# Kernel tuning notes

Hardware: AMD Instinct MI355X
Metric: run time of the kernel (lower is better)

The kernel has to match this reference:

```python
import jax, jax.numpy as jnp
import numpy as np

CURV = 1.0          # Poincare ball curvature c
MIN_NORM = 1e-15    # clamp to avoid div-by-zero
TANH_CLIP = 1.0 - 1e-5  # keep artanh arg < 1


def _mobius_add(x, y, c):
    x2 = jnp.sum(x * x, axis=-1, keepdims=True)
    y2 = jnp.sum(y * y, axis=-1, keepdims=True)
    xy = jnp.sum(x * y, axis=-1, keepdims=True)
    num = (1.0 + 2.0 * c * xy + c * y2) * x + (1.0 - c * x2) * y
    den = 1.0 + 2.0 * c * xy + (c ** 2) * x2 * y2
    return num / jnp.maximum(den, MIN_NORM)


def _logmap(x, y, c):
    """Log map of y in the tangent space at x on the Poincare ball."""
    sub = _mobius_add(-x, y, c)
    sub_norm = jnp.maximum(jnp.linalg.norm(sub, axis=-1, keepdims=True), MIN_NORM)
    x2 = jnp.sum(x * x, axis=-1, keepdims=True)
    lam_x = 2.0 / jnp.maximum(1.0 - c * x2, MIN_NORM)
    sqrt_c = jnp.sqrt(c)
    arg = jnp.clip(sqrt_c * sub_norm, 0.0, TANH_CLIP)
    return (2.0 / (sqrt_c * lam_x)) * jnp.arctanh(arg) * sub / sub_norm


def _expmap(x, v, c):
    """Exp map of tangent vector v at point x on the Poincare ball."""
    v_norm = jnp.maximum(jnp.linalg.norm(v, axis=-1, keepdims=True), MIN_NORM)
    x2 = jnp.sum(x * x, axis=-1, keepdims=True)
    lam_x = 2.0 / jnp.maximum(1.0 - c * x2, MIN_NORM)
    sqrt_c = jnp.sqrt(c)
    second = jnp.tanh(sqrt_c * lam_x * v_norm / 2.0) * v / (sqrt_c * v_norm)
    return _mobius_add(x, second, c)


def setup_inputs() -> dict:
    key = jax.random.key(0)
    k1, k2, k3 = jax.random.split(key, 3)
    N, C_IN, C_OUT = 1536, 64, 64
    # points strictly inside the unit ball (norm ~0.25)
    x = jax.random.normal(k1, (N, C_IN), dtype=jnp.float32) * 0.03
    # Bernoulli(0.02) dense adjacency, float as in the torch module
    adj = (jax.random.uniform(k2, (N, N)) < 0.02).astype(jnp.float32)
    # kaiming-uniform-like init: U(-1/sqrt(fan_in), 1/sqrt(fan_in))
    bound = 1.0 / np.sqrt(C_IN)
    weight = jax.random.uniform(k3, (C_IN, C_OUT), dtype=jnp.float32,
                                minval=-bound, maxval=bound)
    bias = jnp.zeros((C_OUT,), dtype=jnp.float32)
    return {"x": x, "adj": adj, "weight": weight, "bias": bias}


def reference(x, adj, weight, bias):
    c = CURV
    # row-normalized aggregation weights
    deg = jnp.maximum(adj.sum(axis=1, keepdims=True), 1e-8)
    w = adj / deg                                   # (N, N)
    # pairwise logmap: tangent vector at node i pointing toward node j
    log_ij = _logmap(x[:, None, :], x[None, :, :], c)  # (N, N, C_in)
    agg = jnp.einsum('ij,ijc->ic', w, log_ij)          # (N, C_in)
    # (in_channels == out_channels here, so the torch pad/slice branch is a no-op)
    transformed = agg @ weight + bias                  # (N, C_out)
    origin = jnp.zeros_like(transformed)
    return _expmap(origin, transformed, c)
```

## Files before the change

kernel.cpp:

```cpp
#include <hip/hip_runtime.h>
#include <math.h>

#define NN 1536
#define CC 64
#define MAXP 160

__device__ __forceinline__ float wredsum64(float v) {
#pragma unroll
    for (int off = 32; off > 0; off >>= 1) v += __shfl_xor(v, off, 64);
    return v;
}

__launch_bounds__(256, 6)
__global__ void hmp_kernel(const float* __restrict__ x,
                           const float* __restrict__ adj,
                           const float* __restrict__ W,
                           const float* __restrict__ bias,
                           float* __restrict__ out) {
    const int i = blockIdx.x;
    const int tid = threadIdx.x;
    const int w = tid >> 6;
    const int lane = tid & 63;
    const int sub = tid & 15;
    const int g = tid >> 4;

    __shared__ int s_np;
    __shared__ int s_q[MAXP];
    __shared__ float s_qa[MAXP];
    __shared__ float s_part[16][CC];
    __shared__ float s_coefA[16];
    __shared__ float s_deg[4];
    __shared__ float s_agg[CC];
    __shared__ float s_t[4][CC];

    if (tid == 0) s_np = 0;

    const float4 xi4 = reinterpret_cast<const float4*>(x + (size_t)i * CC)[sub];
    const float4* arow4 = reinterpret_cast<const float4*>(adj + (size_t)i * NN);
    const float4 a0 = arow4[tid];
    float4 a1 = make_float4(0.f, 0.f, 0.f, 0.f);
    if (tid < 128) a1 = arow4[256 + tid];

    float a2 = xi4.x * xi4.x + xi4.y * xi4.y + xi4.z * xi4.z + xi4.w * xi4.w;
#pragma unroll
    for (int off = 1; off < 16; off <<= 1) a2 += __shfl_xor(a2, off, 64);
    const float B = 1.0f - a2;

    float degl = a0.x + a0.y + a0.z + a0.w + a1.x + a1.y + a1.z + a1.w;
    degl = wredsum64(degl);
    if (lane == 0) s_deg[w] = degl;

    __syncthreads();

    {
        const float va[8] = {a0.x, a0.y, a0.z, a0.w, a1.x, a1.y, a1.z, a1.w};
#pragma unroll
        for (int k = 0; k < 8; ++k) {
            const float v = va[k];
            if (v != 0.0f) {
                const int p = atomicAdd(&s_np, 1);
                if (p < MAXP) {
                    s_q[p] = (k < 4) ? (4 * tid + k) : (1024 + 4 * tid + (k - 4));
                    s_qa[p] = v;
                }
            }
        }
    }
    __syncthreads();
    const int np = min(s_np, MAXP);

    float accx = 0.f, accy = 0.f, accz = 0.f, accw = 0.f, coefA = 0.f;
    for (int p = g; p < np; p += 16) {
        const int j = s_q[p];
        const float aval = s_qa[p];
        const float4 xj4 = reinterpret_cast<const float4*>(x + (size_t)j * CC)[sub];
        float pd = xi4.x * xj4.x + xi4.y * xj4.y + xi4.z * xj4.z + xi4.w * xj4.w;
        float pb = xj4.x * xj4.x + xj4.y * xj4.y + xj4.z * xj4.z + xj4.w * xj4.w;
#pragma unroll
        for (int off = 1; off < 16; off <<= 1) {
            pd += __shfl_xor(pd, off, 64);
            pb += __shfl_xor(pb, off, 64);
        }
        const float dot = pd, b2 = pb;
        const float A = 1.0f - 2.0f * dot + b2;
        const float D = fmaxf(1.0f - 2.0f * dot + a2 * b2, 1e-15f);
        const float rD = 1.0f / D;
        const float num = fmaxf(A * A * a2 - 2.0f * A * B * dot + B * B * b2, 0.0f);
        const float sub2 = num * rD * rD;
        const float sn = fmaxf(sqrtf(sub2), 1e-15f);
        const float z = fminf(sn, 1.0f - 1e-5f);
        const float ath = 0.5f * logf((1.0f + z) / (1.0f - z));
        const float gg = aval * B * (ath / sn) * rD;
        coefA = fmaf(gg, A, coefA);
        const float gB = gg * B;
        accx = fmaf(gB, xj4.x, accx);
        accy = fmaf(gB, xj4.y, accy);
        accz = fmaf(gB, xj4.z, accz);
        accw = fmaf(gB, xj4.w, accw);
    }
    reinterpret_cast<float4*>(s_part[g])[sub] = make_float4(accx, accy, accz, accw);
    if (sub == 0) s_coefA[g] = coefA;
    __syncthreads();

    if (w == 0) {
        float acct = 0.f, coefAt = 0.f;
#pragma unroll
        for (int q = 0; q < 16; ++q) {
            acct += s_part[q][lane];
            coefAt += s_coefA[q];
        }
        const float deg = fmaxf(s_deg[0] + s_deg[1] + s_deg[2] + s_deg[3], 1e-8f);
        const float xl = x[(size_t)i * CC + lane];
        s_agg[lane] = (acct - xl * coefAt) / deg;
    }
    __syncthreads();

    {
        float t = 0.f;
        const int c0 = w * 16;
#pragma unroll
        for (int k = 0; k < 16; ++k) {
            t = fmaf(s_agg[c0 + k], W[(c0 + k) * CC + lane], t);
        }
        s_t[w][lane] = t;
    }
    __syncthreads();

    if (w == 0) {
        float t = bias[lane] + s_t[0][lane] + s_t[1][lane] + s_t[2][lane] + s_t[3][lane];
        const float vn2 = wredsum64(t * t);
        const float vn = fmaxf(sqrtf(vn2), 1e-15f);
        const float f = tanhf(vn) / vn;
        out[(size_t)i * CC + lane] = f * t;
    }
}

extern "C" void kernel_launch(void* const* d_in, const int* in_sizes, int n_in,
                              void* d_out, int out_size, void* d_ws, size_t ws_size,
                              hipStream_t stream) {
    const float* x    = (const float*)d_in[0];
    const float* adj  = (const float*)d_in[1];
    const float* W    = (const float*)d_in[2];
    const float* bias = (const float*)d_in[3];
    float* out = (float*)d_out;

    hmp_kernel<<<NN, 256, 0, stream>>>(x, adj, W, bias, out);
}
```

Before: 12.44 us.

## Unroll neighbor loop by two, prefetch weights, use fast intrinsics, drop a barrier

The neighbor loop now handles two neighbors per iteration so two gathers and their shuffle reductions can overlap. The weight matrix, bias and x row are loaded into registers at kernel start, before the adjacency scan. Every wave now computes the aggregated vector redundantly, and values are passed by lane shuffle instead of through shared memory, which removes one __syncthreads. Divisions, log and tanh are replaced with hardware reciprocal, __logf and an exp-based tanh, which trades some accuracy for fewer instructions.

```diff
diff --git a/kernel.cpp b/kernel.cpp
--- a/kernel.cpp
+++ b/kernel.cpp
@@ -4,6 +4,8 @@
 #define NN 1536
 #define CC 64
 #define MAXP 160
+
+#define RCP(x) __builtin_amdgcn_rcpf(x)
 
 __device__ __forceinline__ float wredsum64(float v) {
 #pragma unroll
@@ -30,16 +32,22 @@
     __shared__ float s_part[16][CC];
     __shared__ float s_coefA[16];
     __shared__ float s_deg[4];
-    __shared__ float s_agg[CC];
     __shared__ float s_t[4][CC];
 
     if (tid == 0) s_np = 0;
 
-    const float4 xi4 = reinterpret_cast<const float4*>(x + (size_t)i * CC)[sub];
     const float4* arow4 = reinterpret_cast<const float4*>(adj + (size_t)i * NN);
     const float4 a0 = arow4[tid];
     float4 a1 = make_float4(0.f, 0.f, 0.f, 0.f);
     if (tid < 128) a1 = arow4[256 + tid];
+
+    const float4 xi4 = reinterpret_cast<const float4*>(x + (size_t)i * CC)[sub];
+    const float xl = x[(size_t)i * CC + lane];
+    const float bi = bias[lane];
+
+    float wreg[16];
+#pragma unroll
+    for (int k = 0; k < 16; ++k) wreg[k] = W[(size_t)(w * 16 + k) * CC + lane];
 
     float a2 = xi4.x * xi4.x + xi4.y * xi4.y + xi4.z * xi4.z + xi4.w * xi4.w;
 #pragma unroll
@@ -70,68 +78,87 @@
     const int np = min(s_np, MAXP);
 
     float accx = 0.f, accy = 0.f, accz = 0.f, accw = 0.f, coefA = 0.f;
-    for (int p = g; p < np; p += 16) {
-        const int j = s_q[p];
-        const float aval = s_qa[p];
-        const float4 xj4 = reinterpret_cast<const float4*>(x + (size_t)j * CC)[sub];
-        float pd = xi4.x * xj4.x + xi4.y * xj4.y + xi4.z * xj4.z + xi4.w * xj4.w;
-        float pb = xj4.x * xj4.x + xj4.y * xj4.y + xj4.z * xj4.z + xj4.w * xj4.w;
+    for (int p = g; p < np; p += 32) {
+        const int p1 = p + 16;
+        const bool h1 = p1 < np;
+        const int j0 = s_q[p];
+        const float av0 = s_qa[p];
+        const int j1 = h1 ? s_q[p1] : j0;
+        const float av1 = h1 ? s_qa[p1] : 0.0f;
+
+        const float4 xa = reinterpret_cast<const float4*>(x + (size_t)j0 * CC)[sub];
+        const float4 xb = reinterpret_cast<const float4*>(x + (size_t)j1 * CC)[sub];
+
+        float pd0 = xi4.x * xa.x + xi4.y * xa.y + xi4.z * xa.z + xi4.w * xa.w;
+        float pb0 = xa.x * xa.x + xa.y * xa.y + xa.z * xa.z + xa.w * xa.w;
+        float pd1 = xi4.x * xb.x + xi4.y * xb.y + xi4.z * xb.z + xi4.w * xb.w;
+        float pb1 = xb.x * xb.x + xb.y * xb.y + xb.z * xb.z + xb.w * xb.w;
 #pragma unroll
         for (int off = 1; off < 16; off <<= 1) {
-            pd += __shfl_xor(pd, off, 64);
-            pb += __shfl_xor(pb, off, 64);
+            pd0 += __shfl_xor(pd0, off, 64);
+            pb0 += __shfl_xor(pb0, off, 64);
+            pd1 += __shfl_xor(pd1, off, 64);
+            pb1 += __shfl_xor(pb1, off, 64);
         }
-        const float dot = pd, b2 = pb;
-        const float A = 1.0f - 2.0f * dot + b2;
-        const float D = fmaxf(1.0f - 2.0f * dot + a2 * b2, 1e-15f);
-        const float rD = 1.0f / D;
-        const float num = fmaxf(A * A * a2 - 2.0f * A * B * dot + B * B * b2, 0.0f);
-        const float sub2 = num * rD * rD;
-        const float sn = fmaxf(sqrtf(sub2), 1e-15f);
-        const float z = fminf(sn, 1.0f - 1e-5f);
-        const float ath = 0.5f * logf((1.0f + z) / (1.0f - z));
-        const float gg = aval * B * (ath / sn) * rD;
-        coefA = fmaf(gg, A, coefA);
-        const float gB = gg * B;
-        accx = fmaf(gB, xj4.x, accx);
-        accy = fmaf(gB, xj4.y, accy);
-        accz = fmaf(gB, xj4.z, accz);
-        accw = fmaf(gB, xj4.w, accw);
+        {
+            const float A = 1.0f - 2.0f * pd0 + pb0;
+            const float D = fmaxf(1.0f - 2.0f * pd0 + a2 * pb0, 1e-15f);
+            const float rD = RCP(D);
+            const float num = fmaxf(A * A * a2 - 2.0f * A * B * pd0 + B * B * pb0, 0.0f);
+            const float sn = fmaxf(sqrtf(num) * rD, 1e-15f);
+            const float z = fminf(sn, 1.0f - 1e-5f);
+            const float ath = 0.5f * __logf((1.0f + z) * RCP(1.0f - z));
+            const float gg = av0 * B * ath * RCP(sn) * rD;
+            coefA = fmaf(gg, A, coefA);
+            const float gB = gg * B;
+            accx = fmaf(gB, xa.x, accx); accy = fmaf(gB, xa.y, accy);
+            accz = fmaf(gB, xa.z, accz); accw = fmaf(gB, xa.w, accw);
+        }
+        {
+            const float A = 1.0f - 2.0f * pd1 + pb1;
+            const float D = fmaxf(1.0f - 2.0f * pd1 + a2 * pb1, 1e-15f);
+            const float rD = RCP(D);
+            const float num = fmaxf(A * A * a2 - 2.0f * A * B * pd1 + B * B * pb1, 0.0f);
+            const float sn = fmaxf(sqrtf(num) * rD, 1e-15f);
+            const float z = fminf(sn, 1.0f - 1e-5f);
+            const float ath = 0.5f * __logf((1.0f + z) * RCP(1.0f - z));
+            const float gg = av1 * B * ath * RCP(sn) * rD;
+            coefA = fmaf(gg, A, coefA);
+            const float gB = gg * B;
+            accx = fmaf(gB, xb.x, accx); accy = fmaf(gB, xb.y, accy);
+            accz = fmaf(gB, xb.z, accz); accw = fmaf(gB, xb.w, accw);
+        }
     }
     reinterpret_cast<float4*>(s_part[g])[sub] = make_float4(accx, accy, accz, accw);
     if (sub == 0) s_coefA[g] = coefA;
     __syncthreads();
 
-    if (w == 0) {
-        float acct = 0.f, coefAt = 0.f;
+    float acct = 0.f, coefAt = 0.f;
 #pragma unroll
-        for (int q = 0; q < 16; ++q) {
-            acct += s_part[q][lane];
-            coefAt += s_coefA[q];
-        }
-        const float deg = fmaxf(s_deg[0] + s_deg[1] + s_deg[2] + s_deg[3], 1e-8f);
-        const float xl = x[(size_t)i * CC + lane];
-        s_agg[lane] = (acct - xl * coefAt) / deg;
+    for (int q = 0; q < 16; ++q) {
+        acct += s_part[q][lane];
+        coefAt += s_coefA[q];
     }
-    __syncthreads();
+    const float deg = fmaxf(s_deg[0] + s_deg[1] + s_deg[2] + s_deg[3], 1e-8f);
+    const float agg = (acct - xl * coefAt) * RCP(deg);
 
     {
         float t = 0.f;
-        const int c0 = w * 16;
 #pragma unroll
         for (int k = 0; k < 16; ++k) {
-            t = fmaf(s_agg[c0 + k], W[(c0 + k) * CC + lane], t);
+            t = fmaf(__shfl(agg, w * 16 + k, 64), wreg[k], t);
         }
         s_t[w][lane] = t;
     }
     __syncthreads();
 
     if (w == 0) {
-        float t = bias[lane] + s_t[0][lane] + s_t[1][lane] + s_t[2][lane] + s_t[3][lane];
+        float t = bi + s_t[0][lane] + s_t[1][lane] + s_t[2][lane] + s_t[3][lane];
         const float vn2 = wredsum64(t * t);
         const float vn = fmaxf(sqrtf(vn2), 1e-15f);
-        const float f = tanhf(vn) / vn;
-        out[(size_t)i * CC + lane] = f * t;
+        const float e = __expf(2.0f * vn);
+        const float th = 1.0f - 2.0f * RCP(e + 1.0f);
+        out[(size_t)i * CC + lane] = th * RCP(vn) * t;
     }
 }
 
```

Measured after the change: 14.30 us. 15.0% more time.
